# Kernel tuning notes

Hardware: AMD Instinct MI355X
Metric: run time of the kernel (lower is better)

Reference implementation:

```python
import jax, jax.numpy as jnp
import numpy as np

N = 1048576  # total points
B = 64       # number of clouds in batch
D = 64       # feature dim


def _make_lengths():
    rng = np.random.RandomState(0)
    w = rng.rand(B) + 0.5
    lengths = np.floor(w / w.sum() * N).astype(np.int64)
    lengths[-1] += N - lengths.sum()  # make lengths sum exactly to N
    return lengths


def setup_inputs() -> dict:
    key = jax.random.key(0)
    x = jax.random.normal(key, (N, D), dtype=jnp.float32)
    lengths_np = _make_lengths()
    segment_ids = jnp.asarray(np.repeat(np.arange(B, dtype=np.int64), lengths_np))
    lengths = jnp.asarray(lengths_np)
    return {"x": x, "segment_ids": segment_ids, "lengths": lengths}


def reference(x, segment_ids, lengths):
    # fused segmented mean: one pass over x instead of B separate mean kernels
    sums = jax.ops.segment_sum(x, segment_ids, num_segments=B)  # [B, D]
    return sums / lengths.astype(x.dtype)[:, None]
```

## Files before the change

kernel.cpp:

```cpp
#include <hip/hip_runtime.h>


#define D 64
#define ROWS_PER_BLOCK 1024
#define NTHREADS 256

typedef float f32x4 __attribute__((ext_vector_type(4)));

__global__ __launch_bounds__(NTHREADS) void seg_sum_kernel(
    const float* __restrict__ x,
    const int*   __restrict__ seg,
    const int*   __restrict__ len,
    float*       __restrict__ out,
    int n_rows, int B)
{
    __shared__ float l0[4][D];
    __shared__ float l1[4][D];

    const int tid = threadIdx.x;
    const int r0  = blockIdx.x * ROWS_PER_BLOCK;
    if (r0 >= n_rows) return;
    int r1 = r0 + ROWS_PER_BLOCK;
    if (r1 > n_rows) r1 = n_rows;

    const int col     = (tid & 15) * 4;
    const int rowlane = tid >> 4;
    const int lane    = tid & 63;
    const int wid     = tid >> 6;

    const bool full = (r1 - r0) == ROWS_PER_BLOCK;

    int mylen = 0;
    if (B <= 64 && lane < B) mylen = len[lane];

    const float* p = x + (size_t)(r0 + rowlane) * D + col;
    f32x4 w0{}, w1{}, w2{}, w3{}, w4{}, w5{}, w6{}, w7{};
    if (full) {
        w0 = *(const f32x4*)(p + (size_t)0 * 16 * D);
        w1 = *(const f32x4*)(p + (size_t)1 * 16 * D);
        w2 = *(const f32x4*)(p + (size_t)2 * 16 * D);
        w3 = *(const f32x4*)(p + (size_t)3 * 16 * D);
        w4 = *(const f32x4*)(p + (size_t)4 * 16 * D);
        w5 = *(const f32x4*)(p + (size_t)5 * 16 * D);
        w6 = *(const f32x4*)(p + (size_t)6 * 16 * D);
        w7 = *(const f32x4*)(p + (size_t)7 * 16 * D);
    }

    int s0 = 0, nb = 2, boundary = r1;
    if (B <= 64) {
        int incl = mylen;
        #pragma unroll
        for (int d = 1; d < 64; d <<= 1) {
            const int t = __shfl_up(incl, d, 64);
            if (lane >= d) incl += t;
        }
        const int o_beg = incl - mylen;
        s0 = __popcll(__ballot(o_beg <= r0)) - 1;
        const unsigned long long mb = __ballot(o_beg > r0 && o_beg < r1);
        nb = __popcll(mb);
        if (nb) boundary = __shfl(o_beg, (int)(__ffsll((long long)mb) - 1), 64);
    }

    if (nb <= 1) {
        f32x4 a0 = {0.f, 0.f, 0.f, 0.f};
        f32x4 a1 = {0.f, 0.f, 0.f, 0.f};

        if (full && nb == 0) {
            f32x4 t0 = w0, t1 = w1, t2 = w2, t3 = w3;
            t0 += w4; t1 += w5; t2 += w6; t3 += w7;
            #pragma unroll
            for (int it = 1; it < 8; ++it) {
                const float* q = p + (size_t)it * 128 * D;
                const f32x4 v0 = *(const f32x4*)(q + (size_t)0 * 16 * D);
                const f32x4 v1 = *(const f32x4*)(q + (size_t)1 * 16 * D);
                const f32x4 v2 = *(const f32x4*)(q + (size_t)2 * 16 * D);
                const f32x4 v3 = *(const f32x4*)(q + (size_t)3 * 16 * D);
                const f32x4 v4 = *(const f32x4*)(q + (size_t)4 * 16 * D);
                const f32x4 v5 = *(const f32x4*)(q + (size_t)5 * 16 * D);
                const f32x4 v6 = *(const f32x4*)(q + (size_t)6 * 16 * D);
                const f32x4 v7 = *(const f32x4*)(q + (size_t)7 * 16 * D);
                t0 += v0; t1 += v1; t2 += v2; t3 += v3;
                t0 += v4; t1 += v5; t2 += v6; t3 += v7;
            }
            a0 = (t0 + t1) + (t2 + t3);
        } else if (full) {
            const int rbase = r0 + rowlane;
            if (rbase +   0 < boundary) a0 += w0; else a1 += w0;
            if (rbase +  16 < boundary) a0 += w1; else a1 += w1;
            if (rbase +  32 < boundary) a0 += w2; else a1 += w2;
            if (rbase +  48 < boundary) a0 += w3; else a1 += w3;
            if (rbase +  64 < boundary) a0 += w4; else a1 += w4;
            if (rbase +  80 < boundary) a0 += w5; else a1 += w5;
            if (rbase +  96 < boundary) a0 += w6; else a1 += w6;
            if (rbase + 112 < boundary) a0 += w7; else a1 += w7;
            #pragma unroll 8
            for (int r = rbase + 128; r < r1; r += 16) {
                const f32x4 v = *(const f32x4*)(x + (size_t)r * D + col);
                if (r < boundary) { a0 += v; } else { a1 += v; }
            }
        } else {
            for (int r = r0 + rowlane; r < r1; r += 16) {
                const f32x4 v = *(const f32x4*)(x + (size_t)r * D + col);
                if (r < boundary) { a0 += v; } else { a1 += v; }
            }
        }

        #pragma unroll
        for (int j = 0; j < 4; ++j) {
            a0[j] += __shfl_xor(a0[j], 16, 64);
            a0[j] += __shfl_xor(a0[j], 32, 64);
        }
        if (nb) {
            #pragma unroll
            for (int j = 0; j < 4; ++j) {
                a1[j] += __shfl_xor(a1[j], 16, 64);
                a1[j] += __shfl_xor(a1[j], 32, 64);
            }
        }
        if (lane < 16) {
            #pragma unroll
            for (int j = 0; j < 4; ++j) l0[wid][lane * 4 + j] = a0[j];
            if (nb) {
                #pragma unroll
                for (int j = 0; j < 4; ++j) l1[wid][lane * 4 + j] = a1[j];
            }
        }
        __syncthreads();
        if (tid < D) {
            const float s = (l0[0][tid] + l0[1][tid]) + (l0[2][tid] + l0[3][tid]);
            atomicAdd(&out[(size_t)s0 * D + tid], s);
        } else if (nb && tid < 2 * D) {
            const int c = tid - D;
            const float s = (l1[0][c] + l1[1][c]) + (l1[2][c] + l1[3][c]);
            atomicAdd(&out[(size_t)(s0 + 1) * D + c], s);
        }
    } else {
        f32x4 a = {0.f, 0.f, 0.f, 0.f};
        int cur = -1;
        for (int r = r0 + rowlane; r < r1; r += 16) {
            const int s = seg[r];
            const f32x4 v = *(const f32x4*)(x + (size_t)r * D + col);
            if (s != cur) {
                if (cur >= 0) {
                    atomicAdd(&out[(size_t)cur * D + col + 0], a.x);
                    atomicAdd(&out[(size_t)cur * D + col + 1], a.y);
                    atomicAdd(&out[(size_t)cur * D + col + 2], a.z);
                    atomicAdd(&out[(size_t)cur * D + col + 3], a.w);
                }
                a = {0.f, 0.f, 0.f, 0.f};
                cur = s;
            }
            a += v;
        }
        if (cur >= 0) {
            atomicAdd(&out[(size_t)cur * D + col + 0], a.x);
            atomicAdd(&out[(size_t)cur * D + col + 1], a.y);
            atomicAdd(&out[(size_t)cur * D + col + 2], a.z);
            atomicAdd(&out[(size_t)cur * D + col + 3], a.w);
        }
    }
}

__global__ __launch_bounds__(NTHREADS) void seg_div_kernel(
    const int* __restrict__ len,
    float*     __restrict__ out,
    int total)
{
    const int i = blockIdx.x * blockDim.x + threadIdx.x;
    if (i < total) {
        out[i] = out[i] / (float)len[i >> 6];
    }
}

extern "C" void kernel_launch(void* const* d_in, const int* in_sizes, int n_in,
                              void* d_out, int out_size, void* d_ws, size_t ws_size,
                              hipStream_t stream) {
    const float* x   = (const float*)d_in[0];
    const int*   seg = (const int*)d_in[1];
    const int*   len = (const int*)d_in[2];
    float*       out = (float*)d_out;

    const int n_rows = in_sizes[1];
    const int B      = in_sizes[2];
    const int total  = B * D;

    hipMemsetAsync(out, 0, (size_t)total * sizeof(float), stream);

    const int grid = (n_rows + ROWS_PER_BLOCK - 1) / ROWS_PER_BLOCK;
    seg_sum_kernel<<<grid, NTHREADS, 0, stream>>>(x, seg, len, out, n_rows, B);

    const int grid2 = (total + NTHREADS - 1) / NTHREADS;
    seg_div_kernel<<<grid2, NTHREADS, 0, stream>>>(len, out, total);
}
```

Baseline: 357.9 us.

## Fuse mean division into segment-sum kernel and double rows per block

Each partial sum is scaled by the reciprocal of its segment length before the atomic add, so the separate division kernel and its launch go away. Rows per block also double from 1024 to 2048, with the fast-path unroll loop extended to match, halving block count and atomic traffic. The trade-off is fewer blocks in flight for a bandwidth-bound read of x. Per-partial scaling also changes float rounding slightly.

```diff
diff --git a/kernel.cpp b/kernel.cpp
--- a/kernel.cpp
+++ b/kernel.cpp
@@ -2,12 +2,12 @@
 
 
 #define D 64
-#define ROWS_PER_BLOCK 1024
+#define ROWS_PER_BLOCK 2048
 #define NTHREADS 256
 
 typedef float f32x4 __attribute__((ext_vector_type(4)));
 
-__global__ __launch_bounds__(NTHREADS) void seg_sum_kernel(
+__global__ __launch_bounds__(NTHREADS) void seg_mean_kernel(
     const float* __restrict__ x,
     const int*   __restrict__ seg,
     const int*   __restrict__ len,
@@ -47,6 +47,7 @@
     }
 
     int s0 = 0, nb = 2, boundary = r1;
+    float inv0 = 1.0f, inv1 = 1.0f;
     if (B <= 64) {
         int incl = mylen;
         #pragma unroll
@@ -59,6 +60,8 @@
         const unsigned long long mb = __ballot(o_beg > r0 && o_beg < r1);
         nb = __popcll(mb);
         if (nb) boundary = __shfl(o_beg, (int)(__ffsll((long long)mb) - 1), 64);
+        inv0 = 1.0f / (float)__shfl(mylen, s0, 64);
+        if (nb) inv1 = 1.0f / (float)__shfl(mylen, s0 + 1, 64);
     }
 
     if (nb <= 1) {
@@ -69,7 +72,7 @@
             f32x4 t0 = w0, t1 = w1, t2 = w2, t3 = w3;
             t0 += w4; t1 += w5; t2 += w6; t3 += w7;
             #pragma unroll
-            for (int it = 1; it < 8; ++it) {
+            for (int it = 1; it < 16; ++it) {
                 const float* q = p + (size_t)it * 128 * D;
                 const f32x4 v0 = *(const f32x4*)(q + (size_t)0 * 16 * D);
                 const f32x4 v1 = *(const f32x4*)(q + (size_t)1 * 16 * D);
@@ -119,10 +122,10 @@
         }
         if (lane < 16) {
             #pragma unroll
-            for (int j = 0; j < 4; ++j) l0[wid][lane * 4 + j] = a0[j];
+            for (int j = 0; j < 4; ++j) l0[wid][lane * 4 + j] = a0[j] * inv0;
             if (nb) {
                 #pragma unroll
-                for (int j = 0; j < 4; ++j) l1[wid][lane * 4 + j] = a1[j];
+                for (int j = 0; j < 4; ++j) l1[wid][lane * 4 + j] = a1[j] * inv1;
             }
         }
         __syncthreads();
@@ -142,10 +145,11 @@
             const f32x4 v = *(const f32x4*)(x + (size_t)r * D + col);
             if (s != cur) {
                 if (cur >= 0) {
-                    atomicAdd(&out[(size_t)cur * D + col + 0], a.x);
-                    atomicAdd(&out[(size_t)cur * D + col + 1], a.y);
-                    atomicAdd(&out[(size_t)cur * D + col + 2], a.z);
-                    atomicAdd(&out[(size_t)cur * D + col + 3], a.w);
+                    const float inv = 1.0f / (float)len[cur];
+                    atomicAdd(&out[(size_t)cur * D + col + 0], a.x * inv);
+                    atomicAdd(&out[(size_t)cur * D + col + 1], a.y * inv);
+                    atomicAdd(&out[(size_t)cur * D + col + 2], a.z * inv);
+                    atomicAdd(&out[(size_t)cur * D + col + 3], a.w * inv);
                 }
                 a = {0.f, 0.f, 0.f, 0.f};
                 cur = s;
@@ -153,22 +157,12 @@
             a += v;
         }
         if (cur >= 0) {
-            atomicAdd(&out[(size_t)cur * D + col + 0], a.x);
-            atomicAdd(&out[(size_t)cur * D + col + 1], a.y);
-            atomicAdd(&out[(size_t)cur * D + col + 2], a.z);
-            atomicAdd(&out[(size_t)cur * D + col + 3], a.w);
+            const float inv = 1.0f / (float)len[cur];
+            atomicAdd(&out[(size_t)cur * D + col + 0], a.x * inv);
+            atomicAdd(&out[(size_t)cur * D + col + 1], a.y * inv);
+            atomicAdd(&out[(size_t)cur * D + col + 2], a.z * inv);
+            atomicAdd(&out[(size_t)cur * D + col + 3], a.w * inv);
         }
-    }
-}
-
-__global__ __launch_bounds__(NTHREADS) void seg_div_kernel(
-    const int* __restrict__ len,
-    float*     __restrict__ out,
-    int total)
-{
-    const int i = blockIdx.x * blockDim.x + threadIdx.x;
-    if (i < total) {
-        out[i] = out[i] / (float)len[i >> 6];
     }
 }
 
@@ -187,8 +181,5 @@
     hipMemsetAsync(out, 0, (size_t)total * sizeof(float), stream);
 
     const int grid = (n_rows + ROWS_PER_BLOCK - 1) / ROWS_PER_BLOCK;
-    seg_sum_kernel<<<grid, NTHREADS, 0, stream>>>(x, seg, len, out, n_rows, B);
-
-    const int grid2 = (total + NTHREADS - 1) / NTHREADS;
-    seg_div_kernel<<<grid2, NTHREADS, 0, stream>>>(len, out, total);
+    seg_mean_kernel<<<grid, NTHREADS, 0, stream>>>(x, seg, len, out, n_rows, B);
 }
```

New measurement: 361.4 us. About the same (+1.0%).
